# Kernel optimization log

Measured on AMD Instinct MI355X. Metric: run time of the kernel, lower is better.

Reference implementation:

```python
import jax, jax.numpy as jnp
import numpy as np
import math

B, S, DIM = 2, 2048, 2048
H, HD, RD = 16, 128, 64
LKV, LQ = 512, 1536

def _rope(x, cos, sin):
    # x: (B,S,H,RD); interpret consecutive pairs as complex, multiply by e^{i theta}
    b, s, h, d = x.shape
    xr = x.reshape(b, s, h, d // 2, 2)
    xre, xim = xr[..., 0], xr[..., 1]
    c = cos[None, :, None, :]  # (1,S,1,d/2)
    sn = sin[None, :, None, :]
    ore = xre * c - xim * sn
    oim = xre * sn + xim * c
    return jnp.stack([ore, oim], axis=-1).reshape(b, s, h, d)

def setup_inputs() -> dict:
    key = jax.random.key(0)
    ks = jax.random.split(key, 12)
    def w(k, shape, fan_in):
        return jax.random.normal(k, shape, jnp.float32) * (1.0 / math.sqrt(fan_in))
    x = jax.random.normal(ks[0], (B, S, DIM), jnp.float32)
    # RoPE tables for decoupled rotary subspace of width RD
    inv_freq = 1.0 / (10000.0 ** (np.arange(0, RD, 2, dtype=np.float32) / RD))
    ang = np.outer(np.arange(S, dtype=np.float32), inv_freq)  # (S, RD/2)
    freq_cos = jnp.asarray(np.cos(ang), jnp.float32)
    freq_sin = jnp.asarray(np.sin(ang), jnp.float32)
    return {
        "x": x, "freq_cos": freq_cos, "freq_sin": freq_sin,
        "Wkv": w(ks[1], (DIM, LKV), DIM),          # latent_kv (no bias)
        "Wlq": w(ks[2], (DIM, LQ), DIM),           # latent_q (no bias)
        "Wq": w(ks[3], (LQ, H * HD), LQ),          # query (no bias)
        "Wk": w(ks[4], (LKV, H * HD), LKV),        # key (no bias)
        "Wv": w(ks[5], (LKV, H * HD), LKV),        # value (no bias)
        "Wqr": w(ks[6], (LQ, H * RD), LQ),         # decop_rot_q (bias=True)
        "bqr": jnp.zeros((H * RD,), jnp.float32),
        "Wkr": w(ks[7], (DIM, H * RD), DIM),       # decop_rot_k (bias=True)
        "bkr": jnp.zeros((H * RD,), jnp.float32),
        "Wo": w(ks[8], (H * HD, DIM), H * HD),     # out_proj (bias=True)
        "bo": jnp.zeros((DIM,), jnp.float32),
    }

def reference(x, freq_cos, freq_sin, Wkv, Wlq, Wq, Wk, Wv, Wqr, bqr, Wkr, bkr, Wo, bo):
    b, s, _ = x.shape
    cq = x @ Wlq                      # (B,S,LQ)
    ckv = x @ Wkv                     # (B,S,LKV)
    q = (cq @ Wq).reshape(b, s, H, HD)
    qr = _rope((cq @ Wqr + bqr).reshape(b, s, H, RD), freq_cos, freq_sin)
    k = (ckv @ Wk).reshape(b, s, H, HD)
    kr = _rope((x @ Wkr + bkr).reshape(b, s, H, RD), freq_cos, freq_sin)
    v = (ckv @ Wv).reshape(b, s, H, HD)
    qf = jnp.concatenate([q, qr], axis=-1)   # (B,S,H,HD+RD)
    kf = jnp.concatenate([k, kr], axis=-1)
    scale = 1.0 / math.sqrt(HD + RD)
    scores = jnp.einsum('bqhd,bkhd->bhqk', qf, kf) * scale
    # masked=True path: causal tril mask over full seq_len
    mask = jnp.tril(jnp.ones((s, s), bool))
    scores = jnp.where(mask[None, None], scores, -jnp.inf)
    att = jax.nn.softmax(scores.astype(jnp.float32), axis=-1).astype(qf.dtype)
    out = jnp.einsum('bhqk,bkhd->bqhd', att, v).reshape(b, s, H * HD)
    return out @ Wo + bo
```

## Files before the change

kernel.cpp:

```cpp
#include <hip/hip_runtime.h>
#include <hip/hip_bf16.h>
#include <stdint.h>

#define S_LEN 2048
#define NB 2
#define NH 16
#define HDIM 128
#define RDIM 64
#define DF 192
#define MROWS 4096

typedef __bf16 bf16_t;
typedef __attribute__((ext_vector_type(8))) __bf16 bf16x8;
typedef __attribute__((ext_vector_type(4))) __bf16 bf16x4;
typedef __attribute__((ext_vector_type(4))) float f32x4;
typedef __attribute__((ext_vector_type(4))) float float4v;

__device__ __forceinline__ void gload_lds16(const bf16_t* g, bf16_t* l) {
  __builtin_amdgcn_global_load_lds(
      (const __attribute__((address_space(1))) void*)g,
      (__attribute__((address_space(3))) void*)l, 16, 0, 0);
}

__global__ __launch_bounds__(256) void convert_bf16(const float* __restrict__ in,
                                                    bf16_t* __restrict__ out, int n4) {
  int i = blockIdx.x * 256 + threadIdx.x;
  if (i >= n4) return;
  float4v v = *reinterpret_cast<const float4v*>(&in[(size_t)i * 4]);
  bf16x4 o;
  o[0] = (bf16_t)v[0]; o[1] = (bf16_t)v[1]; o[2] = (bf16_t)v[2]; o[3] = (bf16_t)v[3];
  *reinterpret_cast<bf16x4*>(&out[(size_t)i * 4]) = o;
}

struct TrDesc { const float* src; bf16_t* dst; int K; int N; int nbx; int base; };
struct TrPack { TrDesc d[8]; };

__global__ __launch_bounds__(256) void transpose_all(TrPack p) {
  __shared__ float t[64][65];
  const int bid = blockIdx.x;
  int m = 0;
#pragma unroll
  for (int i = 1; i < 8; ++i) m += (bid >= p.d[i].base);
  const TrDesc td = p.d[m];
  const int local = bid - td.base;
  const int n0 = (local % td.nbx) * 64, k0 = (local / td.nbx) * 64;
  const int tx = threadIdx.x & 63, ty = threadIdx.x >> 6;
#pragma unroll
  for (int i = ty; i < 64; i += 4)
    t[i][tx] = td.src[(size_t)(k0 + i) * td.N + n0 + tx];
  __syncthreads();
#pragma unroll
  for (int i = ty; i < 64; i += 4)
    td.dst[(size_t)(n0 + i) * td.K + k0 + tx] = (bf16_t)t[tx][i];
}

struct EpiParams {
  bf16_t* o0;
  bf16_t* o1;
  bf16_t* o2;
  float* outf;
  const float* bias;
  const float* cosb;
  const float* sinb;
};

template <int MODE>
__device__ __forceinline__ void gemm_body(const bf16_t* __restrict__ A,
                                          const bf16_t* __restrict__ Bt,
                                          int N, int K, int m0, int n0,
                                          bf16_t (*Ab)[256 * 64],
                                          bf16_t (*Bb)[256 * 64], EpiParams ep) {
  const int tid = threadIdx.x;
  const int lane = tid & 63, w = tid >> 6;
  const int l15 = lane & 15, lg = lane >> 4;
  const int mw = (w >> 2) * 128, nw = (w & 3) * 64;
  const int nt = K >> 6;

  auto stage = [&](int t, int buf, int j) {
    const int s = (j & 3) * 512 + tid;
    const int row = s >> 3, c = s & 7;
    const int cs = c ^ (row & 7);
    if (j < 4)
      gload_lds16(A + (size_t)(m0 + row) * K + (t << 6) + cs * 8, &Ab[buf][s * 8]);
    else
      gload_lds16(Bt + (size_t)(n0 + row) * K + (t << 6) + cs * 8, &Bb[buf][s * 8]);
  };

  f32x4 acc[8][4] = {};
#pragma unroll
  for (int j = 0; j < 8; ++j) stage(0, 0, j);
  asm volatile("s_waitcnt vmcnt(0)" ::: "memory");
  __builtin_amdgcn_s_barrier();

  for (int t = 0; t < nt; ++t) {
    const int cur = t & 1;
    const bool pf = (t + 1 < nt);
    bf16x8 bfrag[4][2];
#pragma unroll
    for (int p = 0; p < 4; ++p) {
      if (p == 0) {
#pragma unroll
        for (int j = 0; j < 4; ++j)
#pragma unroll
          for (int kk = 0; kk < 2; ++kk) {
            const int r = nw + j * 16 + l15;
            const int c = kk * 4 + lg;
            bfrag[j][kk] = *reinterpret_cast<const bf16x8*>(
                &Bb[cur][r * 64 + ((c ^ (r & 7)) << 3)]);
          }
      }
      bf16x8 afrag[2][2];
#pragma unroll
      for (int di = 0; di < 2; ++di)
#pragma unroll
        for (int kk = 0; kk < 2; ++kk) {
          const int r = mw + (p * 2 + di) * 16 + l15;
          const int c = kk * 4 + lg;
          afrag[di][kk] = *reinterpret_cast<const bf16x8*>(
              &Ab[cur][r * 64 + ((c ^ (r & 7)) << 3)]);
        }
      if (pf) {
        if (p == 0) { stage(t + 1, cur ^ 1, 0); stage(t + 1, cur ^ 1, 1);
                      stage(t + 1, cur ^ 1, 2); stage(t + 1, cur ^ 1, 3); }
        if (p == 1) { stage(t + 1, cur ^ 1, 4); stage(t + 1, cur ^ 1, 5);
                      stage(t + 1, cur ^ 1, 6); stage(t + 1, cur ^ 1, 7); }
      }
      if (p == 3) asm volatile("s_waitcnt vmcnt(0)" ::: "memory");
      __builtin_amdgcn_s_barrier();
      asm volatile("s_waitcnt lgkmcnt(0)" ::: "memory");
      __builtin_amdgcn_sched_barrier(0);
      __builtin_amdgcn_s_setprio(1);
#pragma unroll
      for (int kk = 0; kk < 2; ++kk)
#pragma unroll
        for (int di = 0; di < 2; ++di)
#pragma unroll
          for (int j = 0; j < 4; ++j)
            acc[p * 2 + di][j] = __builtin_amdgcn_mfma_f32_16x16x32_bf16(
                afrag[di][kk], bfrag[j][kk], acc[p * 2 + di][j], 0, 0, 0);
      __builtin_amdgcn_s_setprio(0);
      __builtin_amdgcn_s_barrier();
    }
  }

#pragma unroll
  for (int i = 0; i < 8; ++i)
#pragma unroll
    for (int j = 0; j < 4; ++j) {
      const int col = n0 + nw + j * 16 + l15;
#pragma unroll
      for (int r = 0; r < 4; ++r) {
        const int row = m0 + mw + i * 16 + lg * 4 + r;
        float v = acc[i][j][r];
        const int b = row >> 11, s = row & 2047;
        if constexpr (MODE == 1) {
          ep.outf[(size_t)row * N + col] = v + ep.bias[col];
        } else if constexpr (MODE == 5) {
          if (col < 1536) {
            ep.o0[(size_t)row * 1536 + col] = (bf16_t)v;
          } else if (col < 2048) {
            ep.o1[(size_t)row * 512 + (col - 1536)] = (bf16_t)v;
          } else {
            const int c2 = col - 2048;
            float vb = v + ep.bias[c2];
            float other = __shfl_xor(vb, 1, 64);
            const int h = c2 >> 6, dr = c2 & 63;
            const int fi = dr >> 1;
            const float c = ep.cosb[s * 32 + fi];
            const float sn = ep.sinb[s * 32 + fi];
            const float o = (c2 & 1) ? (other * sn + vb * c) : (vb * c - other * sn);
            ep.o2[(((size_t)(b * NH + h)) * S_LEN + s) * DF + 128 + dr] = (bf16_t)o;
          }
        } else if constexpr (MODE == 6) {
          if (col < 2048) {
            const int h = col >> 7, d = col & 127;
            ep.o0[(((size_t)(b * NH + h)) * S_LEN + s) * DF + d] = (bf16_t)v;
          } else {
            const int c2 = col - 2048;
            float vb = v + ep.bias[c2];
            float other = __shfl_xor(vb, 1, 64);
            const int h = c2 >> 6, dr = c2 & 63;
            const int fi = dr >> 1;
            const float c = ep.cosb[s * 32 + fi];
            const float sn = ep.sinb[s * 32 + fi];
            const float o = (c2 & 1) ? (other * sn + vb * c) : (vb * c - other * sn);
            ep.o0[(((size_t)(b * NH + h)) * S_LEN + s) * DF + 128 + dr] = (bf16_t)o;
          }
        } else {
          if (col < 2048) {
            const int h = col >> 7, d = col & 127;
            ep.o0[(((size_t)(b * NH + h)) * S_LEN + s) * DF + d] = (bf16_t)v;
          } else {
            const int c2 = col - 2048;
            const int h = c2 >> 7, d = c2 & 127;
            ep.o1[(((size_t)(b * NH + h)) * HDIM + d) * S_LEN + s] = (bf16_t)v;
          }
        }
      }
    }
}

template <int MODE>
__global__ __launch_bounds__(512, 2) void gemm_t8(const bf16_t* __restrict__ A,
                                                  const bf16_t* __restrict__ Bt,
                                                  int N, int K, EpiParams ep) {
  __shared__ alignas(16) bf16_t Ab[2][256 * 64];
  __shared__ alignas(16) bf16_t Bb[2][256 * 64];
  const int nwg = gridDim.x;
  int f = blockIdx.x;
  f = (f & 7) * (nwg >> 3) + (f >> 3);
  const int nbx = N >> 8;
  const int m0 = (f / nbx) * 256, n0 = (f % nbx) * 256;
  gemm_body<MODE>(A, Bt, N, K, m0, n0, Ab, Bb, ep);
}

__global__ __launch_bounds__(512, 2) void gemm_t867(const bf16_t* __restrict__ A6,
                                                    const bf16_t* __restrict__ Bt6,
                                                    const bf16_t* __restrict__ A7,
                                                    const bf16_t* __restrict__ Bt7,
                                                    EpiParams ep6, EpiParams ep7) {
  __shared__ alignas(16) bf16_t Ab[2][256 * 64];
  __shared__ alignas(16) bf16_t Bb[2][256 * 64];
  const int bid = blockIdx.x;
  if (bid < 192) {
    int f = (bid & 7) * 24 + (bid >> 3);
    const int m0 = (f / 12) * 256, n0 = (f % 12) * 256;
    gemm_body<6>(A6, Bt6, 3072, 1536, m0, n0, Ab, Bb, ep6);
  } else {
    int b2 = bid - 192;
    int f = (b2 & 7) * 32 + (b2 >> 3);
    const int m0 = (f / 16) * 256, n0 = (f % 16) * 256;
    gemm_body<7>(A7, Bt7, 4096, 512, m0, n0, Ab, Bb, ep7);
  }
}

__global__ __launch_bounds__(256, 2) void attn_fwd(const bf16_t* __restrict__ qf,
                                                   const bf16_t* __restrict__ kf,
                                                   const bf16_t* __restrict__ vT,
                                                   bf16_t* __restrict__ att) {
  const int tid = threadIdx.x;
  const int lane = tid & 63, w = tid >> 6;
  const int l15 = lane & 15, lg = lane >> 4;
  const int l = blockIdx.x;
  const int bh = (l & 7) * 4 + ((l >> 3) & 3);
  const int qchunk = l >> 5;
  const int qb0 = (15 - qchunk) * 128;
  const int q0 = qb0 + w * 32;
  const float scale = 0.07216878364870322f;

  __shared__ alignas(16) bf16_t Ks[64 * 192];
  __shared__ alignas(16) bf16_t Vs[128 * 64];
  __shared__ alignas(16) bf16_t Ps[4 * 2048];

  bf16x8 qfr[2][6];
#pragma unroll
  for (int mf = 0; mf < 2; ++mf) {
    const bf16_t* qptr = qf + ((size_t)bh * S_LEN + q0 + mf * 16 + l15) * DF + lg * 8;
#pragma unroll
    for (int d = 0; d < 6; ++d)
      qfr[mf][d] = *reinterpret_cast<const bf16x8*>(qptr + d * 32);
  }

  f32x4 o[2][8] = {};
  float mrun[2] = {-1e30f, -1e30f}, lsum[2] = {0.0f, 0.0f};

  const bf16_t* kb0 = kf + (size_t)bh * S_LEN * DF;
  const bf16_t* vb0 = vT + (size_t)bh * HDIM * S_LEN;
  const int njt = qb0 / 64 + 2;
  const int wslot = tid & ~63;

  for (int jt = 0; jt < njt; ++jt) {
    const int j0 = jt * 64;
    __syncthreads();
    const bf16_t* kTile = kb0 + (size_t)j0 * DF;
#pragma unroll
    for (int i = 0; i < 6; ++i) {
      const int s = i * 256 + tid;
      const int row = s / 24;
      const int c = s - row * 24;
      const int cs = c ^ (row & 7);
      gload_lds16(kTile + (size_t)row * DF + cs * 8,
                  Ks + (size_t)(i * 256 + wslot) * 8);
    }
    const bf16_t* vTile = vb0 + j0;
#pragma unroll
    for (int i = 0; i < 4; ++i) {
      const int s = i * 256 + tid;
      const int row = s >> 3;
      const int c = s & 7;
      const int cs = c ^ (row & 7);
      gload_lds16(vTile + (size_t)row * S_LEN + cs * 8,
                  Vs + (size_t)(i * 256 + wslot) * 8);
    }
    __syncthreads();

    if (j0 > q0 + 31) continue;

    f32x4 sa[2][4] = {};
    __builtin_amdgcn_s_setprio(1);
#pragma unroll
    for (int jf = 0; jf < 4; ++jf) {
      const int krow = jf * 16 + l15;
      const int ksw = krow & 7;
#pragma unroll
      for (int d = 0; d < 6; ++d) {
        const int kc = (4 * d + lg) ^ ksw;
        bf16x8 kfr = *reinterpret_cast<const bf16x8*>(&Ks[krow * 192 + kc * 8]);
#pragma unroll
        for (int mf = 0; mf < 2; ++mf)
          sa[mf][jf] =
              __builtin_amdgcn_mfma_f32_16x16x32_bf16(kfr, qfr[mf][d], sa[mf][jf], 0, 0, 0);
      }
    }
    __builtin_amdgcn_s_setprio(0);

#pragma unroll
    for (int mf = 0; mf < 2; ++mf) {
      const int qi = q0 + mf * 16 + l15;
      const bool full = (j0 + 63 <= q0 + mf * 16);
      float sv[16];
#pragma unroll
      for (int jf = 0; jf < 4; ++jf)
#pragma unroll
        for (int r = 0; r < 4; ++r) {
          float x = sa[mf][jf][r] * scale;
          if (!full) {
            const int j = j0 + jf * 16 + lg * 4 + r;
            if (j > qi) x = -1e30f;
          }
          sv[jf * 4 + r] = x;
        }

      float a8[8];
#pragma unroll
      for (int i = 0; i < 8; ++i) a8[i] = fmaxf(sv[i], sv[i + 8]);
#pragma unroll
      for (int i = 0; i < 4; ++i) a8[i] = fmaxf(a8[i], a8[i + 4]);
      float mx = fmaxf(fmaxf(a8[0], a8[1]), fmaxf(a8[2], a8[3]));
      mx = fmaxf(mx, __shfl_xor(mx, 16, 64));
      mx = fmaxf(mx, __shfl_xor(mx, 32, 64));

      if (__any(mx > mrun[mf] + 8.0f)) {
        const float mn = fmaxf(mrun[mf], mx);
        const float alpha = __expf(mrun[mf] - mn);
        mrun[mf] = mn;
        lsum[mf] *= alpha;
        float af[4];
#pragma unroll
        for (int r = 0; r < 4; ++r) af[r] = __shfl(alpha, lg * 4 + r, 16);
#pragma unroll
        for (int dt = 0; dt < 8; ++dt)
#pragma unroll
          for (int r = 0; r < 4; ++r) o[mf][dt][r] *= af[r];
      }

#pragma unroll
      for (int i = 0; i < 16; ++i) sv[i] = __expf(sv[i] - mrun[mf]);
      float s8[8];
#pragma unroll
      for (int i = 0; i < 8; ++i) s8[i] = sv[i] + sv[i + 8];
#pragma unroll
      for (int i = 0; i < 4; ++i) s8[i] = s8[i] + s8[i + 4];
      float sm = (s8[0] + s8[1]) + (s8[2] + s8[3]);
      sm += __shfl_xor(sm, 16, 64);
      sm += __shfl_xor(sm, 32, 64);
      lsum[mf] += sm;

#pragma unroll
      for (int jf = 0; jf < 4; ++jf) {
        bf16x4 pk;
#pragma unroll
        for (int r = 0; r < 4; ++r) pk[r] = (bf16_t)sv[jf * 4 + r];
        const int key = jf * 16 + lg * 4;
        *reinterpret_cast<bf16x4*>(
            &Ps[w * 2048 + mf * 1024 + l15 * 64 + (key ^ ((l15 & 7) << 3))]) = pk;
      }
    }
    asm volatile("s_waitcnt lgkmcnt(0)" ::: "memory");
    __builtin_amdgcn_sched_barrier(0);
    bf16x8 pfr[2][2];
#pragma unroll
    for (int mf = 0; mf < 2; ++mf)
#pragma unroll
      for (int jk = 0; jk < 2; ++jk)
        pfr[mf][jk] = *reinterpret_cast<const bf16x8*>(
            &Ps[w * 2048 + mf * 1024 + l15 * 64 + (((jk * 4 + lg) ^ (l15 & 7)) << 3)]);

    __builtin_amdgcn_s_setprio(1);
#pragma unroll
    for (int dt = 0; dt < 8; ++dt) {
      const int vrow = dt * 16 + l15;
      const int vsw = vrow & 7;
#pragma unroll
      for (int jk = 0; jk < 2; ++jk) {
        const int vc = (jk * 4 + lg) ^ vsw;
        bf16x8 vfr = *reinterpret_cast<const bf16x8*>(&Vs[vrow * 64 + vc * 8]);
#pragma unroll
        for (int mf = 0; mf < 2; ++mf)
          o[mf][dt] =
              __builtin_amdgcn_mfma_f32_16x16x32_bf16(pfr[mf][jk], vfr, o[mf][dt], 0, 0, 0);
      }
    }
    __builtin_amdgcn_s_setprio(0);
  }

  const int b = bh >> 4, h = bh & 15;
#pragma unroll
  for (int mf = 0; mf < 2; ++mf) {
    const float inv = 1.0f / lsum[mf];
    float iv[4];
#pragma unroll
    for (int r = 0; r < 4; ++r) iv[r] = __shfl(inv, lg * 4 + r, 16);
#pragma unroll
    for (int dt = 0; dt < 8; ++dt)
#pragma unroll
      for (int r = 0; r < 4; ++r) {
        const int s = q0 + mf * 16 + lg * 4 + r;
        att[((size_t)b * S_LEN + s) * 2048 + h * 128 + dt * 16 + l15] =
            (bf16_t)(o[mf][dt][r] * iv[r]);
      }
  }
}

extern "C" void kernel_launch(void* const* d_in, const int* in_sizes, int n_in,
                              void* d_out, int out_size, void* d_ws, size_t ws_size,
                              hipStream_t stream) {
  const float* x    = (const float*)d_in[0];
  const float* fcos = (const float*)d_in[1];
  const float* fsin = (const float*)d_in[2];
  const float* Wkv  = (const float*)d_in[3];
  const float* Wlq  = (const float*)d_in[4];
  const float* Wq   = (const float*)d_in[5];
  const float* Wk   = (const float*)d_in[6];
  const float* Wv   = (const float*)d_in[7];
  const float* Wqr  = (const float*)d_in[8];
  const float* bqr  = (const float*)d_in[9];
  const float* Wkr  = (const float*)d_in[10];
  const float* bkr  = (const float*)d_in[11];
  const float* Wo   = (const float*)d_in[12];
  const float* bo   = (const float*)d_in[13];
  float* out = (float*)d_out;

  char* ws = (char*)d_ws;
  size_t off = 0;
  auto alloc = [&](size_t bytes) {
    void* p = ws + off;
    off += (bytes + 255) & ~(size_t)255;
    return p;
  };
  bf16_t* xb    = (bf16_t*)alloc((size_t)MROWS * 2048 * 2);
  bf16_t* WcatA = (bf16_t*)alloc((size_t)3072 * 2048 * 2);
  bf16_t* WcatB = (bf16_t*)alloc((size_t)3072 * 1536 * 2);
  bf16_t* WcatC = (bf16_t*)alloc((size_t)4096 * 512 * 2);
  bf16_t* WoT   = (bf16_t*)alloc((size_t)2048 * 2048 * 2);
  bf16_t* cq    = (bf16_t*)alloc((size_t)MROWS * 1536 * 2);
  bf16_t* ckv   = (bf16_t*)alloc((size_t)MROWS * 512 * 2);
  bf16_t* qfb   = (bf16_t*)alloc((size_t)NB * NH * S_LEN * DF * 2);
  bf16_t* kfb   = (bf16_t*)alloc((size_t)NB * NH * S_LEN * DF * 2);
  bf16_t* vTb   = (bf16_t*)alloc((size_t)NB * NH * HDIM * S_LEN * 2);
  bf16_t* attb  = (bf16_t*)alloc((size_t)MROWS * 2048 * 2);

  {
    int n4 = (MROWS * 2048) / 4;
    convert_bf16<<<dim3((n4 + 255) / 256), dim3(256), 0, stream>>>(x, xb, n4);
  }
  {
    TrPack p;
    int base = 0;
    auto set = [&](int i, const float* s, bf16_t* d, int K, int N) {
      p.d[i] = {s, d, K, N, N / 64, base};
      base += (N / 64) * (K / 64);
    };
    set(0, Wlq, WcatA, 2048, 1536);
    set(1, Wkv, WcatA + (size_t)1536 * 2048, 2048, 512);
    set(2, Wkr, WcatA + (size_t)2048 * 2048, 2048, 1024);
    set(3, Wq,  WcatB, 1536, 2048);
    set(4, Wqr, WcatB + (size_t)2048 * 1536, 1536, 1024);
    set(5, Wk,  WcatC, 512, 2048);
    set(6, Wv,  WcatC + (size_t)2048 * 512, 512, 2048);
    set(7, Wo,  WoT, 2048, 2048);
    transpose_all<<<dim3(base), dim3(256), 0, stream>>>(p);
  }

  EpiParams ep{}, ep2{};

  ep = {cq, ckv, kfb, nullptr, bkr, fcos, fsin};
  gemm_t8<5><<<dim3(192), dim3(512), 0, stream>>>(xb, WcatA, 3072, 2048, ep);
  ep  = {qfb, nullptr, nullptr, nullptr, bqr, fcos, fsin};
  ep2 = {kfb, vTb, nullptr, nullptr, nullptr, nullptr, nullptr};
  gemm_t867<<<dim3(448), dim3(512), 0, stream>>>(cq, WcatB, ckv, WcatC, ep, ep2);
  attn_fwd<<<dim3(512), dim3(256), 0, stream>>>(qfb, kfb, vTb, attb);
  ep = {nullptr, nullptr, nullptr, out, bo, nullptr, nullptr};
  gemm_t8<1><<<dim3(128), dim3(512), 0, stream>>>(attb, WoT, 2048, 2048, ep);
}
```

Measured before the change: 380.7 us.

## Restructure GEMM main loop into 8-phase half-tile pipelined schedule

The 256x256 GEMM body is rewritten so A and B tiles are staged as 128-row halves into separate LDS buffers. Each K-step is split into four MFMA phases over sub-quadrants, and the global-to-LDS loads of individual halves are interleaved between phases with partial vmcnt waits. This replaces the old full-tile double buffer that waited on vmcnt(0) every iteration, aiming to hide global load latency behind MFMA work. It adds more barriers per iteration and assumes K is a multiple of 128.

Result: no change. 376.1 us (-1.2%).

```diff
diff --git a/kernel.cpp b/kernel.cpp
--- a/kernel.cpp
+++ b/kernel.cpp
@@ -64,82 +64,120 @@
   const float* sinb;
 };
 
+#define GEMM_MFMA(af, bf, I0, J0)                                              \
+  __builtin_amdgcn_s_barrier();                                                \
+  asm volatile("s_waitcnt lgkmcnt(0)" ::: "memory");                           \
+  __builtin_amdgcn_sched_barrier(0);                                           \
+  __builtin_amdgcn_s_setprio(1);                                               \
+  _Pragma("unroll") for (int kk = 0; kk < 2; ++kk)                             \
+  _Pragma("unroll") for (int i = 0; i < 4; ++i)                                \
+  _Pragma("unroll") for (int j = 0; j < 2; ++j)                                \
+      acc[(I0) + i][(J0) + j] = __builtin_amdgcn_mfma_f32_16x16x32_bf16(       \
+          af[i][kk], bf[j][kk], acc[(I0) + i][(J0) + j], 0, 0, 0);             \
+  __builtin_amdgcn_s_setprio(0);                                               \
+  __builtin_amdgcn_s_barrier();
+
 template <int MODE>
-__device__ __forceinline__ void gemm_body(const bf16_t* __restrict__ A,
-                                          const bf16_t* __restrict__ Bt,
-                                          int N, int K, int m0, int n0,
-                                          bf16_t (*Ab)[256 * 64],
-                                          bf16_t (*Bb)[256 * 64], EpiParams ep) {
+__device__ __forceinline__ void gemm8_body(const bf16_t* __restrict__ A,
+                                           const bf16_t* __restrict__ Bt,
+                                           int N, int K, int m0, int n0,
+                                           bf16_t* __restrict__ Ah,
+                                           bf16_t* __restrict__ Bh,
+                                           EpiParams ep) {
   const int tid = threadIdx.x;
   const int lane = tid & 63, w = tid >> 6;
   const int l15 = lane & 15, lg = lane >> 4;
-  const int mw = (w >> 2) * 128, nw = (w & 3) * 64;
-  const int nt = K >> 6;
-
-  auto stage = [&](int t, int buf, int j) {
-    const int s = (j & 3) * 512 + tid;
-    const int row = s >> 3, c = s & 7;
-    const int cs = c ^ (row & 7);
-    if (j < 4)
-      gload_lds16(A + (size_t)(m0 + row) * K + (t << 6) + cs * 8, &Ab[buf][s * 8]);
-    else
-      gload_lds16(Bt + (size_t)(n0 + row) * K + (t << 6) + cs * 8, &Bb[buf][s * 8]);
+  const int mg = w >> 2, ng = w & 3;
+  const int mw = mg * 128, nw = ng * 64;
+  const int bbase = (ng & 1) * 64;
+  const int niter = K >> 7;
+
+  auto stageHalf = [&](int kt, int u) {
+    const int db = kt & 1;
+    const int kof = kt << 6;
+#pragma unroll
+    for (int i = 0; i < 2; ++i) {
+      const int s = i * 512 + tid;
+      const int row = s >> 3, c = s & 7;
+      const int cs = c ^ (row & 7);
+      if (u == 0)
+        gload_lds16(A + (size_t)(m0 + row) * K + kof + cs * 8,
+                    Ah + (size_t)(db * 2 + 0) * 8192 + s * 8);
+      else if (u == 1)
+        gload_lds16(A + (size_t)(m0 + 128 + row) * K + kof + cs * 8,
+                    Ah + (size_t)(db * 2 + 1) * 8192 + s * 8);
+      else if (u == 2)
+        gload_lds16(Bt + (size_t)(n0 + row) * K + kof + cs * 8,
+                    Bh + (size_t)(db * 2 + 0) * 8192 + s * 8);
+      else
+        gload_lds16(Bt + (size_t)(n0 + 128 + row) * K + kof + cs * 8,
+                    Bh + (size_t)(db * 2 + 1) * 8192 + s * 8);
+    }
   };
+  auto readA = [&](int db, int msub, bf16x8 a[4][2]) {
+    const bf16_t* base = Ah + (size_t)(db * 2 + mg) * 8192;
+#pragma unroll
+    for (int i = 0; i < 4; ++i) {
+      const int lrow = msub * 64 + i * 16 + l15;
+#pragma unroll
+      for (int kk = 0; kk < 2; ++kk) {
+        const int c = kk * 4 + lg;
+        a[i][kk] = *reinterpret_cast<const bf16x8*>(
+            base + lrow * 64 + ((c ^ (lrow & 7)) << 3));
+      }
+    }
+  };
+  auto readB = [&](int db, int nh, bf16x8 b[2][2]) {
+    const bf16_t* base = Bh + (size_t)(db * 2 + (ng >> 1)) * 8192;
+#pragma unroll
+    for (int j = 0; j < 2; ++j) {
+      const int lrow = bbase + (nh * 2 + j) * 16 + l15;
+#pragma unroll
+      for (int kk = 0; kk < 2; ++kk) {
+        const int c = kk * 4 + lg;
+        b[j][kk] = *reinterpret_cast<const bf16x8*>(
+            base + lrow * 64 + ((c ^ (lrow & 7)) << 3));
+      }
+    }
+  };
 
   f32x4 acc[8][4] = {};
-#pragma unroll
-  for (int j = 0; j < 8; ++j) stage(0, 0, j);
-  asm volatile("s_waitcnt vmcnt(0)" ::: "memory");
+  stageHalf(0, 0); stageHalf(0, 1); stageHalf(0, 2); stageHalf(0, 3);
+  stageHalf(1, 2); stageHalf(1, 3); stageHalf(1, 0);
+  asm volatile("s_waitcnt vmcnt(6)" ::: "memory");
   __builtin_amdgcn_s_barrier();
 
-  for (int t = 0; t < nt; ++t) {
-    const int cur = t & 1;
-    const bool pf = (t + 1 < nt);
-    bf16x8 bfrag[4][2];
-#pragma unroll
-    for (int p = 0; p < 4; ++p) {
-      if (p == 0) {
-#pragma unroll
-        for (int j = 0; j < 4; ++j)
-#pragma unroll
-          for (int kk = 0; kk < 2; ++kk) {
-            const int r = nw + j * 16 + l15;
-            const int c = kk * 4 + lg;
-            bfrag[j][kk] = *reinterpret_cast<const bf16x8*>(
-                &Bb[cur][r * 64 + ((c ^ (r & 7)) << 3)]);
-          }
-      }
-      bf16x8 afrag[2][2];
-#pragma unroll
-      for (int di = 0; di < 2; ++di)
-#pragma unroll
-        for (int kk = 0; kk < 2; ++kk) {
-          const int r = mw + (p * 2 + di) * 16 + l15;
-          const int c = kk * 4 + lg;
-          afrag[di][kk] = *reinterpret_cast<const bf16x8*>(
-              &Ab[cur][r * 64 + ((c ^ (r & 7)) << 3)]);
-        }
+  for (int t = 0; t < niter; ++t) {
+    const bool pf = (t + 1 < niter);
+    const int ke = 2 * t + 2, ko = 2 * t + 3;
+
+#pragma unroll
+    for (int half = 0; half < 2; ++half) {
+      const int db = half;
+      const int nx = (half == 0) ? ke : ko;
+      bf16x8 a0[4][2], a1[4][2], b0[2][2], b1[2][2];
+
+      readA(db, 0, a0);
+      readB(db, 0, b0);
+      if (half == 0) stageHalf(2 * t + 1, 1);
+      else if (pf) stageHalf(ke, 1);
+      GEMM_MFMA(a0, b0, 0, 0)
+
+      readB(db, 1, b1);
+      if (pf) stageHalf(nx, 2);
+      GEMM_MFMA(a0, b1, 0, 2)
+
+      readA(db, 1, a1);
+      if (pf) stageHalf(nx, 3);
+      GEMM_MFMA(a1, b1, 4, 2)
+
       if (pf) {
-        if (p == 0) { stage(t + 1, cur ^ 1, 0); stage(t + 1, cur ^ 1, 1);
-                      stage(t + 1, cur ^ 1, 2); stage(t + 1, cur ^ 1, 3); }
-        if (p == 1) { stage(t + 1, cur ^ 1, 4); stage(t + 1, cur ^ 1, 5);
-                      stage(t + 1, cur ^ 1, 6); stage(t + 1, cur ^ 1, 7); }
-      }
-      if (p == 3) asm volatile("s_waitcnt vmcnt(0)" ::: "memory");
-      __builtin_amdgcn_s_barrier();
-      asm volatile("s_waitcnt lgkmcnt(0)" ::: "memory");
-      __builtin_amdgcn_sched_barrier(0);
-      __builtin_amdgcn_s_setprio(1);
-#pragma unroll
-      for (int kk = 0; kk < 2; ++kk)
-#pragma unroll
-        for (int di = 0; di < 2; ++di)
-#pragma unroll
-          for (int j = 0; j < 4; ++j)
-            acc[p * 2 + di][j] = __builtin_amdgcn_mfma_f32_16x16x32_bf16(
-                afrag[di][kk], bfrag[j][kk], acc[p * 2 + di][j], 0, 0, 0);
-      __builtin_amdgcn_s_setprio(0);
-      __builtin_amdgcn_s_barrier();
+        stageHalf(nx, 0);
+        asm volatile("s_waitcnt vmcnt(6)" ::: "memory");
+      } else {
+        asm volatile("s_waitcnt vmcnt(0)" ::: "memory");
+      }
+      GEMM_MFMA(a1, b0, 4, 0)
     }
   }
 
@@ -201,36 +239,36 @@
 }
 
 template <int MODE>
-__global__ __launch_bounds__(512, 2) void gemm_t8(const bf16_t* __restrict__ A,
-                                                  const bf16_t* __restrict__ Bt,
-                                                  int N, int K, EpiParams ep) {
-  __shared__ alignas(16) bf16_t Ab[2][256 * 64];
-  __shared__ alignas(16) bf16_t Bb[2][256 * 64];
+__global__ __launch_bounds__(512, 2) void gemm_8ph(const bf16_t* __restrict__ A,
+                                                   const bf16_t* __restrict__ Bt,
+                                                   int N, int K, EpiParams ep) {
+  __shared__ alignas(16) bf16_t Ah[2 * 2 * 8192];
+  __shared__ alignas(16) bf16_t Bh[2 * 2 * 8192];
   const int nwg = gridDim.x;
   int f = blockIdx.x;
   f = (f & 7) * (nwg >> 3) + (f >> 3);
   const int nbx = N >> 8;
   const int m0 = (f / nbx) * 256, n0 = (f % nbx) * 256;
-  gemm_body<MODE>(A, Bt, N, K, m0, n0, Ab, Bb, ep);
-}
-
-__global__ __launch_bounds__(512, 2) void gemm_t867(const bf16_t* __restrict__ A6,
-                                                    const bf16_t* __restrict__ Bt6,
-                                                    const bf16_t* __restrict__ A7,
-                                                    const bf16_t* __restrict__ Bt7,
-                                                    EpiParams ep6, EpiParams ep7) {
-  __shared__ alignas(16) bf16_t Ab[2][256 * 64];
-  __shared__ alignas(16) bf16_t Bb[2][256 * 64];
+  gemm8_body<MODE>(A, Bt, N, K, m0, n0, Ah, Bh, ep);
+}
+
+__global__ __launch_bounds__(512, 2) void gemm_8ph67(const bf16_t* __restrict__ A6,
+                                                     const bf16_t* __restrict__ Bt6,
+                                                     const bf16_t* __restrict__ A7,
+                                                     const bf16_t* __restrict__ Bt7,
+                                                     EpiParams ep6, EpiParams ep7) {
+  __shared__ alignas(16) bf16_t Ah[2 * 2 * 8192];
+  __shared__ alignas(16) bf16_t Bh[2 * 2 * 8192];
   const int bid = blockIdx.x;
   if (bid < 192) {
     int f = (bid & 7) * 24 + (bid >> 3);
     const int m0 = (f / 12) * 256, n0 = (f % 12) * 256;
-    gemm_body<6>(A6, Bt6, 3072, 1536, m0, n0, Ab, Bb, ep6);
+    gemm8_body<6>(A6, Bt6, 3072, 1536, m0, n0, Ah, Bh, ep6);
   } else {
     int b2 = bid - 192;
     int f = (b2 & 7) * 32 + (b2 >> 3);
     const int m0 = (f / 16) * 256, n0 = (f % 16) * 256;
-    gemm_body<7>(A7, Bt7, 4096, 512, m0, n0, Ab, Bb, ep7);
+    gemm8_body<7>(A7, Bt7, 4096, 512, m0, n0, Ah, Bh, ep7);
   }
 }
 
@@ -485,11 +523,11 @@
   EpiParams ep{}, ep2{};
 
   ep = {cq, ckv, kfb, nullptr, bkr, fcos, fsin};
-  gemm_t8<5><<<dim3(192), dim3(512), 0, stream>>>(xb, WcatA, 3072, 2048, ep);
+  gemm_8ph<5><<<dim3(192), dim3(512), 0, stream>>>(xb, WcatA, 3072, 2048, ep);
   ep  = {qfb, nullptr, nullptr, nullptr, bqr, fcos, fsin};
   ep2 = {kfb, vTb, nullptr, nullptr, nullptr, nullptr, nullptr};
-  gemm_t867<<<dim3(448), dim3(512), 0, stream>>>(cq, WcatB, ckv, WcatC, ep, ep2);
+  gemm_8ph67<<<dim3(448), dim3(512), 0, stream>>>(cq, WcatB, ckv, WcatC, ep, ep2);
   attn_fwd<<<dim3(512), dim3(256), 0, stream>>>(qfb, kfb, vTb, attb);
   ep = {nullptr, nullptr, nullptr, out, bo, nullptr, nullptr};
-  gemm_t8<1><<<dim3(128), dim3(512), 0, stream>>>(attb, WoT, 2048, 2048, ep);
-}
+  gemm_8ph<1><<<dim3(128), dim3(512), 0, stream>>>(attb, WoT, 2048, 2048, ep);
+}
```
